# Kernel optimization log

Measured on AMD Instinct MI355X. Metric: run time of the kernel, lower is better.

## Reference

```python
import jax, jax.numpy as jnp
import numpy as np

B, HR, WR, C, HEADS, WS = 32, 64, 64, 128, 4, 8
HD = C // HEADS            # head dim = 32
N = WS * WS                # tokens per window = 64
NB = (2 * WS - 1) ** 2     # relative-bias table rows = 225
EPS = 1e-5


def _relative_bias_index():
    # Static int index, identical to SwinMSA._get_relative_bias_index
    coords = np.stack(np.meshgrid(np.arange(WS), np.arange(WS), indexing='ij'))  # (2, ws, ws)
    flat = coords.reshape(2, -1)                      # (2, n)
    rel = flat[:, :, None] - flat[:, None, :]         # (2, n, n)
    rel = rel.transpose(1, 2, 0).copy()               # (n, n, 2)
    rel[:, :, 0] += WS - 1
    rel[:, :, 1] += WS - 1
    rel[:, :, 0] *= 2 * WS - 1
    return rel.sum(-1)                                # (n, n) int

_REL_IDX = _relative_bias_index()


def _ln(x, g, b):
    m = jnp.mean(x, axis=-1, keepdims=True)
    v = jnp.mean(jnp.square(x - m), axis=-1, keepdims=True)
    return (x - m) * jax.lax.rsqrt(v + EPS) * g + b


def setup_inputs() -> dict:
    key = jax.random.key(0)
    ks = jax.random.split(key, 16)
    s = 0.02
    return {
        'x': jax.random.normal(ks[0], (B, HR * WR, C), jnp.float32),
        'qkv_w': jax.random.normal(ks[1], (C, 3 * C), jnp.float32) * s,
        'qkv_b': jnp.zeros((3 * C,), jnp.float32),
        'proj_w': jax.random.normal(ks[2], (C, C), jnp.float32) * s,
        'proj_b': jnp.zeros((C,), jnp.float32),
        'rel_bias_table': jax.random.normal(ks[3], (NB, HEADS), jnp.float32) * s,
        'ln1_g': jnp.ones((C,), jnp.float32),
        'ln1_b': jnp.zeros((C,), jnp.float32),
        'ln2_g': jnp.ones((C,), jnp.float32),
        'ln2_b': jnp.zeros((C,), jnp.float32),
        'mlp_w1': jax.random.normal(ks[4], (C, 4 * C), jnp.float32) * s,
        'mlp_b1': jnp.zeros((4 * C,), jnp.float32),
        'mlp_w2': jax.random.normal(ks[5], (4 * C, C), jnp.float32) * s,
        'mlp_b2': jnp.zeros((C,), jnp.float32),
    }


def reference(x, qkv_w, qkv_b, proj_w, proj_b, rel_bias_table,
              ln1_g, ln1_b, ln2_g, ln2_b, mlp_w1, mlp_b1, mlp_w2, mlp_b2):
    b = x.shape[0]
    hb, wb = HR // WS, WR // WS
    img = x.reshape(b, HR, WR, C)
    n1 = _ln(img, ln1_g, ln1_b)
    # window_partition: '(wy h) (wx w)' split puts window coord OUTER (strided windows),
    # faithful to the source rearrange.
    part = n1.reshape(b, WS, hb, WS, wb, C).transpose(0, 2, 4, 1, 3, 5)
    part = part.reshape(b * hb * wb, N, C)            # (Bw, n, c)
    qkv = part @ qkv_w + qkv_b                        # (Bw, n, 3c)
    # rearrange 'b n (h d c) -> d b n h c': channel factors as (head, 3, head_dim)
    qkv = qkv.reshape(-1, N, HEADS, 3, HD)
    q, k, v = qkv[..., 0, :], qkv[..., 1, :], qkv[..., 2, :]   # (Bw, n, h, hd)
    energy = jnp.einsum('bqhe,bkhe->bqhk', q, k) * (HD ** -0.5)
    bias = rel_bias_table[_REL_IDX.reshape(-1)].reshape(N, N, HEADS)
    bias = bias.transpose(2, 0, 1)                    # (h, n, n)
    energy = energy + bias.transpose(1, 0, 2)[None]   # broadcast as (q, h, k)
    attn = jax.nn.softmax(energy, axis=-1)
    out = jnp.einsum('bihv,bvhd->bihd', attn, v).reshape(-1, N, C)
    out = out @ proj_w + proj_b                       # (Bw, n, c)
    # window_reverse (inverse of the strided partition)
    rev = out.reshape(b, hb, wb, WS, WS, C).transpose(0, 3, 1, 4, 2, 5)
    rev = rev.reshape(b, HR * WR, C)
    msa = x + rev
    h2 = _ln(msa, ln2_g, ln2_b)
    mlp = jax.nn.gelu(h2 @ mlp_w1 + mlp_b1, approximate=False) @ mlp_w2 + mlp_b2
    return msa + mlp
```

## Files before the change

kernel.cpp:

```cpp
#include <hip/hip_runtime.h>

typedef __attribute__((ext_vector_type(4))) float f32x4;
typedef __attribute__((ext_vector_type(8))) short bf16x8;
typedef __attribute__((ext_vector_type(4))) short bf16x4;
typedef unsigned short u16;

__device__ __forceinline__ u16 f2bf(float f){
  unsigned u = __float_as_uint(f);
  u += 0x7FFFu + ((u >> 16) & 1u);
  return (u16)(u >> 16);
}

__global__ void repack_kernel(const float* __restrict__ qkv_w, const float* __restrict__ proj_w,
                              const float* __restrict__ w1, const float* __restrict__ w2,
                              const float* __restrict__ tbl,
                              u16* __restrict__ rq, u16* __restrict__ rp,
                              u16* __restrict__ r1, u16* __restrict__ r2,
                              float* __restrict__ be){
  const int i = blockIdx.x * 256 + threadIdx.x;
  const int j = i & 7, lane = (i >> 3) & 63, f = i >> 9;
  const int kr = (lane >> 4) * 8 + j;
  const int c16 = lane & 15;
  if (i < 49152){ int nt = f % 24, kk = f / 24; rq[i] = f2bf(qkv_w[(kk*32 + kr)*384 + nt*16 + c16]); }
  if (i < 16384){ int nt = f & 7,  kk = f >> 3; rp[i] = f2bf(proj_w[(kk*32 + kr)*128 + nt*16 + c16]); }
  if (i < 65536){ int nt = f & 31, kk = f >> 5; r1[i] = f2bf(w1[(kk*32 + kr)*512 + nt*16 + c16]); }
  if (i < 65536){ int nt = f & 7,  kk = f >> 3; r2[i] = f2bf(w2[(kk*32 + kr)*128 + nt*16 + c16]); }
  if (i < 16384){
    int rg = i & 3, ln = (i >> 2) & 63, g = i >> 8;
    int nt = g & 3, mt = (g >> 2) & 3, h = g >> 4;
    int row = mt*16 + (ln >> 4)*4 + rg;
    int col = nt*16 + (ln & 15);
    int rel = ((col >> 3) - (row >> 3) + 7) * 15 + ((col & 7) - (row & 7) + 7);
    be[i] = tbl[rel*4 + h];
  }
}

__global__ __launch_bounds__(256, 2)
void block_kernel(const float* __restrict__ x,
                  const float* __restrict__ qkv_b, const float* __restrict__ proj_b,
                  const float* __restrict__ ln1_g, const float* __restrict__ ln1_b,
                  const float* __restrict__ ln2_g, const float* __restrict__ ln2_b,
                  const u16* __restrict__ rep_qkv, const u16* __restrict__ rep_proj,
                  const u16* __restrict__ rep_w1, const u16* __restrict__ rep_w2,
                  const float* __restrict__ mlp_b1, const float* __restrict__ mlp_b2,
                  const float* __restrict__ bias_exp,
                  float* __restrict__ out){
  __shared__ __align__(16) u16 smem[32768];
  u16* sLN = smem;
  u16* sQ  = smem + 8192;
  u16* sK  = smem + 16384;
  u16* sV  = smem + 24576;
  u16* sP  = smem + 8192;
  u16* sO  = smem;
  u16* sH  = smem;
  u16* sG  = smem + 24576;
  float* stg = (float*)(smem + 8192);

  const int tid = threadIdx.x, lane = tid & 63, wid = tid >> 6;
  const int wdw = blockIdx.x;
  const int bb = wdw >> 6, ihb = (wdw >> 3) & 7, iwb = wdw & 7;
  const float* xb = x + (size_t)bb * 4096 * 128;
  float* ob = out + (size_t)bb * 4096 * 128;
  const f32x4 z4 = {0.f, 0.f, 0.f, 0.f};
  const int rb = tid >> 4, cb = tid & 15, c0g = cb * 8;
  const int r15 = lane & 15, kg = lane >> 4;
  float xs[4][8];

  {
    float g8[8], b8[8];
    *(f32x4*)&g8[0] = *(const f32x4*)(ln1_g + c0g);
    *(f32x4*)&g8[4] = *(const f32x4*)(ln1_g + c0g + 4);
    *(f32x4*)&b8[0] = *(const f32x4*)(ln1_b + c0g);
    *(f32x4*)&b8[4] = *(const f32x4*)(ln1_b + c0g + 4);
    #pragma unroll
    for (int it = 0; it < 4; ++it){
      const int r = it * 16 + rb;
      const int pix = ((r >> 3) * 8 + ihb) * 64 + (r & 7) * 8 + iwb;
      *(f32x4*)&xs[it][0] = *(const f32x4*)(xb + (size_t)pix * 128 + c0g);
      *(f32x4*)&xs[it][4] = *(const f32x4*)(xb + (size_t)pix * 128 + c0g + 4);
      float s = 0.f, sq = 0.f;
      #pragma unroll
      for (int j = 0; j < 8; ++j){ s += xs[it][j]; sq += xs[it][j]*xs[it][j]; }
      #pragma unroll
      for (int m = 1; m < 16; m <<= 1){ s += __shfl_xor(s, m); sq += __shfl_xor(sq, m); }
      const float mean = s * (1.f/128.f);
      const float rs = rsqrtf(sq * (1.f/128.f) - mean*mean + 1e-5f);
      bf16x8 o;
      #pragma unroll
      for (int j = 0; j < 8; ++j)
        o[j] = (short)f2bf((xs[it][j]-mean)*rs*g8[j] + b8[j]);
      *(bf16x8*)&sLN[r*128 + (c0g ^ ((r & 7) << 3))] = o;
    }
  }
  __syncthreads();

  {
    f32x4 aqk[4][4];
    f32x4 av[4][2];
    #pragma unroll
    for (int ct = 0; ct < 4; ++ct){
      const f32x4 bq = *(const f32x4*)(qkv_b + wid*96 + ct*16 + kg*4);
      #pragma unroll
      for (int tt = 0; tt < 4; ++tt) aqk[ct][tt] = bq;
    }
    #pragma unroll
    for (int nt = 0; nt < 2; ++nt){
      const float bv = qkv_b[wid*96 + 64 + nt*16 + r15];
      const f32x4 bv4 = {bv, bv, bv, bv};
      #pragma unroll
      for (int mt = 0; mt < 4; ++mt) av[mt][nt] = bv4;
    }
    #pragma unroll
    for (int kk = 0; kk < 4; ++kk){
      bf16x8 L[4], aW[4], bWv[2];
      const int c0 = kk*32 + kg*8;
      #pragma unroll
      for (int t = 0; t < 4; ++t){
        const int row = t*16 + r15;
        L[t] = *(const bf16x8*)&sLN[row*128 + (c0 ^ ((row & 7) << 3))];
      }
      #pragma unroll
      for (int ct = 0; ct < 4; ++ct)
        aW[ct] = *(const bf16x8*)(rep_qkv + (size_t)((kk*24 + wid*6 + ct)*64 + lane)*8);
      #pragma unroll
      for (int nt = 0; nt < 2; ++nt)
        bWv[nt] = *(const bf16x8*)(rep_qkv + (size_t)((kk*24 + wid*6 + 4 + nt)*64 + lane)*8);
      #pragma unroll
      for (int ct = 0; ct < 4; ++ct)
        #pragma unroll
        for (int tt = 0; tt < 4; ++tt)
          aqk[ct][tt] = __builtin_amdgcn_mfma_f32_16x16x32_bf16(aW[ct], L[tt], aqk[ct][tt], 0, 0, 0);
      #pragma unroll
      for (int mt = 0; mt < 4; ++mt)
        #pragma unroll
        for (int nt = 0; nt < 2; ++nt)
          av[mt][nt] = __builtin_amdgcn_mfma_f32_16x16x32_bf16(L[mt], bWv[nt], av[mt][nt], 0, 0, 0);
    }
    #pragma unroll
    for (int ct = 0; ct < 4; ++ct){
      u16* dst = (ct < 2) ? sQ : sK;
      const float scl = (ct < 2) ? 0.17677669529663687f : 1.0f;
      const int colu = wid*32 + (ct & 1)*16 + kg*4;
      #pragma unroll
      for (int tt = 0; tt < 4; ++tt){
        const int row = tt*16 + r15;
        bf16x4 pk;
        #pragma unroll
        for (int rg = 0; rg < 4; ++rg) pk[rg] = (short)f2bf(aqk[ct][tt][rg] * scl);
        *(bf16x4*)&dst[row*128 + (colu ^ ((row & 7) << 3))] = pk;
      }
    }
    #pragma unroll
    for (int nt = 0; nt < 2; ++nt){
      const int row = wid*32 + nt*16 + r15;
      #pragma unroll
      for (int mt = 0; mt < 4; ++mt){
        const int colu = mt*16 + kg*4;
        bf16x4 pk;
        #pragma unroll
        for (int rg = 0; rg < 4; ++rg) pk[rg] = (short)f2bf(av[mt][nt][rg]);
        *(bf16x4*)&sV[row*64 + (colu ^ ((row & 7) << 3))] = pk;
      }
    }
  }
  __syncthreads();

  f32x4 s4[4][4];
  {
    bf16x8 aK[4], bQ[4];
    #pragma unroll
    for (int t = 0; t < 4; ++t){
      const int row = t*16 + r15;
      const int off = (wid*32 + kg*8) ^ ((row & 7) << 3);
      aK[t] = *(const bf16x8*)&sK[row*128 + off];
      bQ[t] = *(const bf16x8*)&sQ[row*128 + off];
    }
    #pragma unroll
    for (int mtk = 0; mtk < 4; ++mtk)
      #pragma unroll
      for (int ntq = 0; ntq < 4; ++ntq){
        const f32x4 cb4 = *(const f32x4*)(bias_exp + (size_t)(((wid*4 + mtk)*4 + ntq)*64 + lane)*4);
        s4[mtk][ntq] = __builtin_amdgcn_mfma_f32_16x16x32_bf16(aK[mtk], bQ[ntq], cb4, 0, 0, 0);
      }
  }
  #pragma unroll
  for (int ntq = 0; ntq < 4; ++ntq){
    float mx = s4[0][ntq][0];
    #pragma unroll
    for (int mtk = 0; mtk < 4; ++mtk)
      #pragma unroll
      for (int rg = 0; rg < 4; ++rg) mx = fmaxf(mx, s4[mtk][ntq][rg]);
    mx = fmaxf(mx, __shfl_xor(mx, 16));
    mx = fmaxf(mx, __shfl_xor(mx, 32));
    float sum = 0.f;
    #pragma unroll
    for (int mtk = 0; mtk < 4; ++mtk)
      #pragma unroll
      for (int rg = 0; rg < 4; ++rg){
        const float e = __expf(s4[mtk][ntq][rg] - mx);
        s4[mtk][ntq][rg] = e; sum += e;
      }
    sum += __shfl_xor(sum, 16);
    sum += __shfl_xor(sum, 32);
    const float inv = __builtin_amdgcn_rcpf(sum);
    #pragma unroll
    for (int mtk = 0; mtk < 4; ++mtk)
      #pragma unroll
      for (int rg = 0; rg < 4; ++rg) s4[mtk][ntq][rg] *= inv;
  }
  __syncthreads();
  #pragma unroll
  for (int ntq = 0; ntq < 4; ++ntq){
    const int row = ntq*16 + r15;
    #pragma unroll
    for (int mtk = 0; mtk < 4; ++mtk){
      const int colu = wid*64 + mtk*16 + kg*4;
      bf16x4 pk;
      #pragma unroll
      for (int rg = 0; rg < 4; ++rg) pk[rg] = (short)f2bf(s4[mtk][ntq][rg]);
      *(bf16x4*)&sP[row*256 + (colu ^ ((row & 7) << 3))] = pk;
    }
  }
  __syncthreads();

  {
    f32x4 o4[2][4];
    #pragma unroll
    for (int dt = 0; dt < 2; ++dt)
      #pragma unroll
      for (int qt = 0; qt < 4; ++qt) o4[dt][qt] = z4;
    #pragma unroll
    for (int ks = 0; ks < 2; ++ks){
      bf16x8 aV[2], bP[4];
      #pragma unroll
      for (int dt = 0; dt < 2; ++dt){
        const int rowd = wid*32 + dt*16 + r15;
        aV[dt] = *(const bf16x8*)&sV[rowd*64 + ((ks*32 + kg*8) ^ ((rowd & 7) << 3))];
      }
      #pragma unroll
      for (int qt = 0; qt < 4; ++qt){
        const int rowq = qt*16 + r15;
        bP[qt] = *(const bf16x8*)&sP[rowq*256 + ((wid*64 + ks*32 + kg*8) ^ ((rowq & 7) << 3))];
      }
      #pragma unroll
      for (int dt = 0; dt < 2; ++dt)
        #pragma unroll
        for (int qt = 0; qt < 4; ++qt)
          o4[dt][qt] = __builtin_amdgcn_mfma_f32_16x16x32_bf16(aV[dt], bP[qt], o4[dt][qt], 0, 0, 0);
    }
    #pragma unroll
    for (int dt = 0; dt < 2; ++dt){
      const int dbase = wid*32 + dt*16 + kg*4;
      #pragma unroll
      for (int qt = 0; qt < 4; ++qt){
        const int q = qt*16 + r15;
        bf16x4 pk;
        #pragma unroll
        for (int rg = 0; rg < 4; ++rg) pk[rg] = (short)f2bf(o4[dt][qt][rg]);
        *(bf16x4*)&sO[q*128 + (dbase ^ ((q & 7) << 3))] = pk;
      }
    }
  }
  __syncthreads();

  {
    f32x4 po[2][4];
    #pragma unroll
    for (int ot = 0; ot < 2; ++ot){
      const f32x4 pb4 = *(const f32x4*)(proj_b + (wid*2 + ot)*16 + kg*4);
      #pragma unroll
      for (int tt = 0; tt < 4; ++tt) po[ot][tt] = pb4;
    }
    #pragma unroll
    for (int kk = 0; kk < 4; ++kk){
      bf16x8 aWp[2], bO[4];
      #pragma unroll
      for (int ot = 0; ot < 2; ++ot)
        aWp[ot] = *(const bf16x8*)(rep_proj + (size_t)((kk*8 + wid*2 + ot)*64 + lane)*8);
      #pragma unroll
      for (int tt = 0; tt < 4; ++tt){
        const int row = tt*16 + r15;
        bO[tt] = *(const bf16x8*)&sO[row*128 + ((kk*32 + kg*8) ^ ((row & 7) << 3))];
      }
      #pragma unroll
      for (int ot = 0; ot < 2; ++ot)
        #pragma unroll
        for (int tt = 0; tt < 4; ++tt)
          po[ot][tt] = __builtin_amdgcn_mfma_f32_16x16x32_bf16(aWp[ot], bO[tt], po[ot][tt], 0, 0, 0);
    }
    #pragma unroll
    for (int ot = 0; ot < 2; ++ot){
      const int cbase = (wid*2 + ot)*16 + kg*4;
      #pragma unroll
      for (int tt = 0; tt < 4; ++tt){
        const int tok = tt*16 + r15;
        *(f32x4*)&stg[tok*128 + (cbase ^ ((tok & 7) << 2))] = po[ot][tt];
      }
    }
  }
  __syncthreads();

  {
    float g8[8], b8[8];
    *(f32x4*)&g8[0] = *(const f32x4*)(ln2_g + c0g);
    *(f32x4*)&g8[4] = *(const f32x4*)(ln2_g + c0g + 4);
    *(f32x4*)&b8[0] = *(const f32x4*)(ln2_b + c0g);
    *(f32x4*)&b8[4] = *(const f32x4*)(ln2_b + c0g + 4);
    #pragma unroll
    for (int it = 0; it < 4; ++it){
      const int r = it * 16 + rb;
      const int m4 = (r & 7) << 2;
      f32x4 p0 = *(const f32x4*)&stg[r*128 + (c0g ^ m4)];
      f32x4 p1 = *(const f32x4*)&stg[r*128 + ((c0g + 4) ^ m4)];
      float ms[8];
      #pragma unroll
      for (int j = 0; j < 4; ++j){ ms[j] = xs[it][j] + p0[j]; ms[4+j] = xs[it][4+j] + p1[j]; }
      #pragma unroll
      for (int j = 0; j < 4; ++j){ p0[j] = ms[j]; p1[j] = ms[4+j]; }
      *(f32x4*)&stg[r*128 + (c0g ^ m4)] = p0;
      *(f32x4*)&stg[r*128 + ((c0g + 4) ^ m4)] = p1;
      float s = 0.f, sq = 0.f;
      #pragma unroll
      for (int j = 0; j < 8; ++j){ s += ms[j]; sq += ms[j]*ms[j]; }
      #pragma unroll
      for (int m = 1; m < 16; m <<= 1){ s += __shfl_xor(s, m); sq += __shfl_xor(sq, m); }
      const float mean = s * (1.f/128.f);
      const float rs = rsqrtf(sq * (1.f/128.f) - mean*mean + 1e-5f);
      bf16x8 o;
      #pragma unroll
      for (int j = 0; j < 8; ++j)
        o[j] = (short)f2bf((ms[j]-mean)*rs*g8[j] + b8[j]);
      *(bf16x8*)&sH[r*128 + (c0g ^ ((r & 7) << 3))] = o;
    }
  }
  __syncthreads();

  f32x4 accO[2][4];
  #pragma unroll
  for (int ot = 0; ot < 2; ++ot){
    const f32x4 b2v = *(const f32x4*)(mlp_b2 + (wid*2 + ot)*16 + kg*4);
    #pragma unroll
    for (int tt = 0; tt < 4; ++tt) accO[ot][tt] = b2v;
  }
  #pragma unroll
  for (int c = 0; c < 4; ++c){
    f32x4 t4[2][4];
    #pragma unroll
    for (int ht = 0; ht < 2; ++ht){
      const f32x4 b1v = *(const f32x4*)(mlp_b1 + c*128 + (wid*2 + ht)*16 + kg*4);
      #pragma unroll
      for (int tt = 0; tt < 4; ++tt) t4[ht][tt] = b1v;
    }
    #pragma unroll
    for (int kk = 0; kk < 4; ++kk){
      bf16x8 aW[2], bL[4];
      const int c0 = kk*32 + kg*8;
      #pragma unroll
      for (int ht = 0; ht < 2; ++ht)
        aW[ht] = *(const bf16x8*)(rep_w1 + (size_t)((kk*32 + c*8 + wid*2 + ht)*64 + lane)*8);
      #pragma unroll
      for (int tt = 0; tt < 4; ++tt){
        const int row = tt*16 + r15;
        bL[tt] = *(const bf16x8*)&sH[row*128 + (c0 ^ ((row & 7) << 3))];
      }
      #pragma unroll
      for (int ht = 0; ht < 2; ++ht)
        #pragma unroll
        for (int tt = 0; tt < 4; ++tt)
          t4[ht][tt] = __builtin_amdgcn_mfma_f32_16x16x32_bf16(aW[ht], bL[tt], t4[ht][tt], 0, 0, 0);
    }
    bf16x4 gp[2][4];
    #pragma unroll
    for (int ht = 0; ht < 2; ++ht)
      #pragma unroll
      for (int tt = 0; tt < 4; ++tt){
        #pragma unroll
        for (int rg = 0; rg < 4; ++rg){
          const float v = t4[ht][tt][rg];
          const float e = __expf(-1.702f * v);
          gp[ht][tt][rg] = (short)f2bf(v * __builtin_amdgcn_rcpf(1.f + e));
        }
      }
    __syncthreads();
    #pragma unroll
    for (int ht = 0; ht < 2; ++ht){
      const int colu = (wid*2 + ht)*16 + kg*4;
      #pragma unroll
      for (int tt = 0; tt < 4; ++tt){
        const int row = tt*16 + r15;
        *(bf16x4*)&sG[row*128 + (colu ^ ((row & 7) << 3))] = gp[ht][tt];
      }
    }
    __syncthreads();
    #pragma unroll
    for (int kk = 0; kk < 4; ++kk){
      bf16x8 aW2[2], bG[4];
      const int c0 = kk*32 + kg*8;
      #pragma unroll
      for (int ot = 0; ot < 2; ++ot)
        aW2[ot] = *(const bf16x8*)(rep_w2 + (size_t)(((c*4 + kk)*8 + wid*2 + ot)*64 + lane)*8);
      #pragma unroll
      for (int tt = 0; tt < 4; ++tt){
        const int row = tt*16 + r15;
        bG[tt] = *(const bf16x8*)&sG[row*128 + (c0 ^ ((row & 7) << 3))];
      }
      #pragma unroll
      for (int ot = 0; ot < 2; ++ot)
        #pragma unroll
        for (int tt = 0; tt < 4; ++tt)
          accO[ot][tt] = __builtin_amdgcn_mfma_f32_16x16x32_bf16(aW2[ot], bG[tt], accO[ot][tt], 0, 0, 0);
    }
  }
  __syncthreads();

  #pragma unroll
  for (int ot = 0; ot < 2; ++ot){
    const int cbase = (wid*2 + ot)*16 + kg*4;
    #pragma unroll
    for (int tt = 0; tt < 4; ++tt){
      const int tok = tt*16 + r15;
      const int pix = ((tok >> 3) * 8 + ihb) * 64 + (tok & 7) * 8 + iwb;
      const f32x4 m4 = *(const f32x4*)&stg[tok*128 + (cbase ^ ((tok & 7) << 2))];
      f32x4 o;
      #pragma unroll
      for (int rg = 0; rg < 4; ++rg) o[rg] = m4[rg] + accO[ot][tt][rg];
      *(f32x4*)(ob + (size_t)pix * 128 + cbase) = o;
    }
  }
}

extern "C" void kernel_launch(void* const* d_in, const int* in_sizes, int n_in,
                              void* d_out, int out_size, void* d_ws, size_t ws_size,
                              hipStream_t stream){
  (void)in_sizes; (void)n_in; (void)out_size; (void)ws_size;
  const float* x      = (const float*)d_in[0];
  const float* qkv_w  = (const float*)d_in[1];
  const float* qkv_b  = (const float*)d_in[2];
  const float* proj_w = (const float*)d_in[3];
  const float* proj_b = (const float*)d_in[4];
  const float* tbl    = (const float*)d_in[5];
  const float* ln1_g  = (const float*)d_in[6];
  const float* ln1_b  = (const float*)d_in[7];
  const float* ln2_g  = (const float*)d_in[8];
  const float* ln2_b  = (const float*)d_in[9];
  const float* w1     = (const float*)d_in[10];
  const float* b1     = (const float*)d_in[11];
  const float* w2     = (const float*)d_in[12];
  const float* b2     = (const float*)d_in[13];

  char* ws = (char*)d_ws;
  u16*   rq  = (u16*)ws;
  u16*   rp  = (u16*)(ws + 98304);
  u16*   r1  = (u16*)(ws + 131072);
  u16*   r2  = (u16*)(ws + 262144);
  float* be  = (float*)(ws + 393216);

  hipLaunchKernelGGL(repack_kernel, dim3(256), dim3(256), 0, stream,
                     qkv_w, proj_w, w1, w2, tbl, rq, rp, r1, r2, be);
  hipLaunchKernelGGL(block_kernel, dim3(2048), dim3(256), 0, stream,
                     x, qkv_b, proj_b, ln1_g, ln1_b, ln2_g, ln2_b,
                     rq, rp, r1, r2, b1, b2, be, (float*)d_out);
}
```

Baseline: 122.2 us.

## Shrink LDS to 48KB with bf16 residual staging for three blocks per CU

Reorganizes shared-memory aliasing so the block uses 48KB instead of 64KB, and stores the attention-residual sum in bf16 rather than fp32. It re-reads x from global memory in the projection epilogue, so the x registers no longer have to stay live across the kernel. Launch bounds rise to 3 blocks per SM. It also folds log2e into the Q scale and the bias so the kernels can use exp2, and swaps in hardware rsq and the library bf16 conversion. The cost is an extra global read of x, added barriers, and a bf16-rounded residual feeding LN2 and the final output, which lowers accuracy.

```diff
diff --git a/kernel.cpp b/kernel.cpp
--- a/kernel.cpp
+++ b/kernel.cpp
@@ -1,15 +1,21 @@
 #include <hip/hip_runtime.h>
+#include <hip/hip_bf16.h>
 
 typedef __attribute__((ext_vector_type(4))) float f32x4;
 typedef __attribute__((ext_vector_type(8))) short bf16x8;
 typedef __attribute__((ext_vector_type(4))) short bf16x4;
+typedef __attribute__((ext_vector_type(2))) unsigned u32x2;
 typedef unsigned short u16;
 
-__device__ __forceinline__ u16 f2bf(float f){
-  unsigned u = __float_as_uint(f);
-  u += 0x7FFFu + ((u >> 16) & 1u);
-  return (u16)(u >> 16);
+__device__ __forceinline__ short fbf(float f){
+  __hip_bfloat16 h = __float2bfloat16(f);
+  return *reinterpret_cast<short*>(&h);
 }
+__device__ __forceinline__ float bf2f(short s){
+  return __uint_as_float(((unsigned)(unsigned short)s) << 16);
+}
+
+#define LOG2E 1.4426950408889634f
 
 __global__ void repack_kernel(const float* __restrict__ qkv_w, const float* __restrict__ proj_w,
                               const float* __restrict__ w1, const float* __restrict__ w2,
@@ -21,21 +27,21 @@
   const int j = i & 7, lane = (i >> 3) & 63, f = i >> 9;
   const int kr = (lane >> 4) * 8 + j;
   const int c16 = lane & 15;
-  if (i < 49152){ int nt = f % 24, kk = f / 24; rq[i] = f2bf(qkv_w[(kk*32 + kr)*384 + nt*16 + c16]); }
-  if (i < 16384){ int nt = f & 7,  kk = f >> 3; rp[i] = f2bf(proj_w[(kk*32 + kr)*128 + nt*16 + c16]); }
-  if (i < 65536){ int nt = f & 31, kk = f >> 5; r1[i] = f2bf(w1[(kk*32 + kr)*512 + nt*16 + c16]); }
-  if (i < 65536){ int nt = f & 7,  kk = f >> 3; r2[i] = f2bf(w2[(kk*32 + kr)*128 + nt*16 + c16]); }
+  if (i < 49152){ int nt = f % 24, kk = f / 24; rq[i] = (u16)fbf(qkv_w[(kk*32 + kr)*384 + nt*16 + c16]); }
+  if (i < 16384){ int nt = f & 7,  kk = f >> 3; rp[i] = (u16)fbf(proj_w[(kk*32 + kr)*128 + nt*16 + c16]); }
+  if (i < 65536){ int nt = f & 31, kk = f >> 5; r1[i] = (u16)fbf(w1[(kk*32 + kr)*512 + nt*16 + c16]); }
+  if (i < 65536){ int nt = f & 7,  kk = f >> 3; r2[i] = (u16)fbf(w2[(kk*32 + kr)*128 + nt*16 + c16]); }
   if (i < 16384){
     int rg = i & 3, ln = (i >> 2) & 63, g = i >> 8;
     int nt = g & 3, mt = (g >> 2) & 3, h = g >> 4;
     int row = mt*16 + (ln >> 4)*4 + rg;
     int col = nt*16 + (ln & 15);
     int rel = ((col >> 3) - (row >> 3) + 7) * 15 + ((col & 7) - (row & 7) + 7);
-    be[i] = tbl[rel*4 + h];
+    be[i] = tbl[rel*4 + h] * LOG2E;
   }
 }
 
-__global__ __launch_bounds__(256, 2)
+__global__ __launch_bounds__(256, 3)
 void block_kernel(const float* __restrict__ x,
                   const float* __restrict__ qkv_b, const float* __restrict__ proj_b,
                   const float* __restrict__ ln1_g, const float* __restrict__ ln1_b,
@@ -45,16 +51,16 @@
                   const float* __restrict__ mlp_b1, const float* __restrict__ mlp_b2,
                   const float* __restrict__ bias_exp,
                   float* __restrict__ out){
-  __shared__ __align__(16) u16 smem[32768];
+  __shared__ __align__(16) u16 smem[24576];
   u16* sLN = smem;
-  u16* sQ  = smem + 8192;
-  u16* sK  = smem + 16384;
-  u16* sV  = smem + 24576;
-  u16* sP  = smem + 8192;
+  u16* sQ  = smem;
+  u16* sK  = smem + 8192;
+  u16* sV  = smem + 16384;
+  u16* sP  = smem;
   u16* sO  = smem;
-  u16* sH  = smem;
-  u16* sG  = smem + 24576;
-  float* stg = (float*)(smem + 8192);
+  u16* stg = smem + 8192;
+  u16* sH  = smem + 16384;
+  u16* sG  = smem;
 
   const int tid = threadIdx.x, lane = tid & 63, wid = tid >> 6;
   const int wdw = blockIdx.x;
@@ -64,7 +70,6 @@
   const f32x4 z4 = {0.f, 0.f, 0.f, 0.f};
   const int rb = tid >> 4, cb = tid & 15, c0g = cb * 8;
   const int r15 = lane & 15, kg = lane >> 4;
-  float xs[4][8];
 
   {
     float g8[8], b8[8];
@@ -76,19 +81,19 @@
     for (int it = 0; it < 4; ++it){
       const int r = it * 16 + rb;
       const int pix = ((r >> 3) * 8 + ihb) * 64 + (r & 7) * 8 + iwb;
-      *(f32x4*)&xs[it][0] = *(const f32x4*)(xb + (size_t)pix * 128 + c0g);
-      *(f32x4*)&xs[it][4] = *(const f32x4*)(xb + (size_t)pix * 128 + c0g + 4);
+      float fl[8];
+      *(f32x4*)&fl[0] = *(const f32x4*)(xb + (size_t)pix * 128 + c0g);
+      *(f32x4*)&fl[4] = *(const f32x4*)(xb + (size_t)pix * 128 + c0g + 4);
       float s = 0.f, sq = 0.f;
       #pragma unroll
-      for (int j = 0; j < 8; ++j){ s += xs[it][j]; sq += xs[it][j]*xs[it][j]; }
+      for (int j = 0; j < 8; ++j){ s += fl[j]; sq += fl[j]*fl[j]; }
       #pragma unroll
       for (int m = 1; m < 16; m <<= 1){ s += __shfl_xor(s, m); sq += __shfl_xor(sq, m); }
       const float mean = s * (1.f/128.f);
-      const float rs = rsqrtf(sq * (1.f/128.f) - mean*mean + 1e-5f);
+      const float rs = __builtin_amdgcn_rsqf(sq * (1.f/128.f) - mean*mean + 1e-5f);
       bf16x8 o;
       #pragma unroll
-      for (int j = 0; j < 8; ++j)
-        o[j] = (short)f2bf((xs[it][j]-mean)*rs*g8[j] + b8[j]);
+      for (int j = 0; j < 8; ++j) o[j] = fbf((fl[j]-mean)*rs*g8[j] + b8[j]);
       *(bf16x8*)&sLN[r*128 + (c0g ^ ((r & 7) << 3))] = o;
     }
   }
@@ -136,17 +141,18 @@
         for (int nt = 0; nt < 2; ++nt)
           av[mt][nt] = __builtin_amdgcn_mfma_f32_16x16x32_bf16(L[mt], bWv[nt], av[mt][nt], 0, 0, 0);
     }
+    __syncthreads();
     #pragma unroll
     for (int ct = 0; ct < 4; ++ct){
       u16* dst = (ct < 2) ? sQ : sK;
-      const float scl = (ct < 2) ? 0.17677669529663687f : 1.0f;
+      const float scl = (ct < 2) ? 0.2550348296f : 1.0f;
       const int colu = wid*32 + (ct & 1)*16 + kg*4;
       #pragma unroll
       for (int tt = 0; tt < 4; ++tt){
         const int row = tt*16 + r15;
         bf16x4 pk;
         #pragma unroll
-        for (int rg = 0; rg < 4; ++rg) pk[rg] = (short)f2bf(aqk[ct][tt][rg] * scl);
+        for (int rg = 0; rg < 4; ++rg) pk[rg] = fbf(aqk[ct][tt][rg] * scl);
         *(bf16x4*)&dst[row*128 + (colu ^ ((row & 7) << 3))] = pk;
       }
     }
@@ -158,7 +164,7 @@
         const int colu = mt*16 + kg*4;
         bf16x4 pk;
         #pragma unroll
-        for (int rg = 0; rg < 4; ++rg) pk[rg] = (short)f2bf(av[mt][nt][rg]);
+        for (int rg = 0; rg < 4; ++rg) pk[rg] = fbf(av[mt][nt][rg]);
         *(bf16x4*)&sV[row*64 + (colu ^ ((row & 7) << 3))] = pk;
       }
     }
@@ -197,7 +203,7 @@
     for (int mtk = 0; mtk < 4; ++mtk)
       #pragma unroll
       for (int rg = 0; rg < 4; ++rg){
-        const float e = __expf(s4[mtk][ntq][rg] - mx);
+        const float e = __builtin_amdgcn_exp2f(s4[mtk][ntq][rg] - mx);
         s4[mtk][ntq][rg] = e; sum += e;
       }
     sum += __shfl_xor(sum, 16);
@@ -214,11 +220,11 @@
     const int row = ntq*16 + r15;
     #pragma unroll
     for (int mtk = 0; mtk < 4; ++mtk){
-      const int colu = wid*64 + mtk*16 + kg*4;
+      const int colu = mtk*16 + kg*4;
       bf16x4 pk;
       #pragma unroll
-      for (int rg = 0; rg < 4; ++rg) pk[rg] = (short)f2bf(s4[mtk][ntq][rg]);
-      *(bf16x4*)&sP[row*256 + (colu ^ ((row & 7) << 3))] = pk;
+      for (int rg = 0; rg < 4; ++rg) pk[rg] = fbf(s4[mtk][ntq][rg]);
+      *(bf16x4*)&sP[wid*4096 + row*64 + (colu ^ ((row & 7) << 3))] = pk;
     }
   }
   __syncthreads();
@@ -240,7 +246,7 @@
       #pragma unroll
       for (int qt = 0; qt < 4; ++qt){
         const int rowq = qt*16 + r15;
-        bP[qt] = *(const bf16x8*)&sP[rowq*256 + ((wid*64 + ks*32 + kg*8) ^ ((rowq & 7) << 3))];
+        bP[qt] = *(const bf16x8*)&sP[wid*4096 + rowq*64 + ((ks*32 + kg*8) ^ ((rowq & 7) << 3))];
       }
       #pragma unroll
       for (int dt = 0; dt < 2; ++dt)
@@ -248,6 +254,7 @@
         for (int qt = 0; qt < 4; ++qt)
           o4[dt][qt] = __builtin_amdgcn_mfma_f32_16x16x32_bf16(aV[dt], bP[qt], o4[dt][qt], 0, 0, 0);
     }
+    __syncthreads();
     #pragma unroll
     for (int dt = 0; dt < 2; ++dt){
       const int dbase = wid*32 + dt*16 + kg*4;
@@ -256,7 +263,7 @@
         const int q = qt*16 + r15;
         bf16x4 pk;
         #pragma unroll
-        for (int rg = 0; rg < 4; ++rg) pk[rg] = (short)f2bf(o4[dt][qt][rg]);
+        for (int rg = 0; rg < 4; ++rg) pk[rg] = fbf(o4[dt][qt][rg]);
         *(bf16x4*)&sO[q*128 + (dbase ^ ((q & 7) << 3))] = pk;
       }
     }
@@ -294,7 +301,12 @@
       #pragma unroll
       for (int tt = 0; tt < 4; ++tt){
         const int tok = tt*16 + r15;
-        *(f32x4*)&stg[tok*128 + (cbase ^ ((tok & 7) << 2))] = po[ot][tt];
+        const int pix = ((tok >> 3) * 8 + ihb) * 64 + (tok & 7) * 8 + iwb;
+        const f32x4 xv = *(const f32x4*)(xb + (size_t)pix * 128 + cbase);
+        bf16x4 pk;
+        #pragma unroll
+        for (int rg = 0; rg < 4; ++rg) pk[rg] = fbf(po[ot][tt][rg] + xv[rg]);
+        *(bf16x4*)&stg[tok*128 + (cbase ^ ((tok & 7) << 3))] = pk;
       }
     }
   }
@@ -309,27 +321,20 @@
     #pragma unroll
     for (int it = 0; it < 4; ++it){
       const int r = it * 16 + rb;
-      const int m4 = (r & 7) << 2;
-      f32x4 p0 = *(const f32x4*)&stg[r*128 + (c0g ^ m4)];
-      f32x4 p1 = *(const f32x4*)&stg[r*128 + ((c0g + 4) ^ m4)];
-      float ms[8];
-      #pragma unroll
-      for (int j = 0; j < 4; ++j){ ms[j] = xs[it][j] + p0[j]; ms[4+j] = xs[it][4+j] + p1[j]; }
-      #pragma unroll
-      for (int j = 0; j < 4; ++j){ p0[j] = ms[j]; p1[j] = ms[4+j]; }
-      *(f32x4*)&stg[r*128 + (c0g ^ m4)] = p0;
-      *(f32x4*)&stg[r*128 + ((c0g + 4) ^ m4)] = p1;
+      bf16x8 m8 = *(const bf16x8*)&stg[r*128 + (c0g ^ ((r & 7) << 3))];
+      float fl[8];
+      #pragma unroll
+      for (int j = 0; j < 8; ++j) fl[j] = bf2f(m8[j]);
       float s = 0.f, sq = 0.f;
       #pragma unroll
-      for (int j = 0; j < 8; ++j){ s += ms[j]; sq += ms[j]*ms[j]; }
+      for (int j = 0; j < 8; ++j){ s += fl[j]; sq += fl[j]*fl[j]; }
       #pragma unroll
       for (int m = 1; m < 16; m <<= 1){ s += __shfl_xor(s, m); sq += __shfl_xor(sq, m); }
       const float mean = s * (1.f/128.f);
-      const float rs = rsqrtf(sq * (1.f/128.f) - mean*mean + 1e-5f);
+      const float rs = __builtin_amdgcn_rsqf(sq * (1.f/128.f) - mean*mean + 1e-5f);
       bf16x8 o;
       #pragma unroll
-      for (int j = 0; j < 8; ++j)
-        o[j] = (short)f2bf((ms[j]-mean)*rs*g8[j] + b8[j]);
+      for (int j = 0; j < 8; ++j) o[j] = fbf((fl[j]-mean)*rs*g8[j] + b8[j]);
       *(bf16x8*)&sH[r*128 + (c0g ^ ((r & 7) << 3))] = o;
     }
   }
@@ -377,8 +382,8 @@
         #pragma unroll
         for (int rg = 0; rg < 4; ++rg){
           const float v = t4[ht][tt][rg];
-          const float e = __expf(-1.702f * v);
-          gp[ht][tt][rg] = (short)f2bf(v * __builtin_amdgcn_rcpf(1.f + e));
+          const float e = __builtin_amdgcn_exp2f(-2.4554669f * v);
+          gp[ht][tt][rg] = fbf(v * __builtin_amdgcn_rcpf(1.f + e));
         }
       }
     __syncthreads();
@@ -411,7 +416,6 @@
           accO[ot][tt] = __builtin_amdgcn_mfma_f32_16x16x32_bf16(aW2[ot], bG[tt], accO[ot][tt], 0, 0, 0);
     }
   }
-  __syncthreads();
 
   #pragma unroll
   for (int ot = 0; ot < 2; ++ot){
@@ -420,10 +424,10 @@
     for (int tt = 0; tt < 4; ++tt){
       const int tok = tt*16 + r15;
       const int pix = ((tok >> 3) * 8 + ihb) * 64 + (tok & 7) * 8 + iwb;
-      const f32x4 m4 = *(const f32x4*)&stg[tok*128 + (cbase ^ ((tok & 7) << 2))];
+      bf16x4 m4 = *(const bf16x4*)&stg[tok*128 + (cbase ^ ((tok & 7) << 3))];
       f32x4 o;
       #pragma unroll
-      for (int rg = 0; rg < 4; ++rg) o[rg] = m4[rg] + accO[ot][tt][rg];
+      for (int rg = 0; rg < 4; ++rg) o[rg] = bf2f(m4[rg]) + accO[ot][tt][rg];
       *(f32x4*)(ob + (size_t)pix * 128 + cbase) = o;
     }
   }
```

New measurement: 98.73 us. 19.2% less time.
